# Performance work log

Hardware: AMD Instinct MI355X
Metric: run time of the kernel (lower is better)

The kernel has to match this reference:

```python
import jax, jax.numpy as jnp
import numpy as np

B, S, D, H = 4, 1024, 1024, 16
DH = D // H  # head dim = 64


def setup_inputs() -> dict:
    key = jax.random.key(0)
    k0, k1, k2 = jax.random.split(key, 3)
    x = jax.random.normal(k0, (B, S, D), dtype=jnp.float32)
    c_attn_w = jax.random.normal(k1, (D, 3 * D), dtype=jnp.float32) * 0.02
    c_attn_b = jnp.zeros((3 * D,), dtype=jnp.float32)
    c_proj_w = jax.random.normal(k2, (D, D), dtype=jnp.float32) * 0.02
    c_proj_b = jnp.zeros((D,), dtype=jnp.float32)
    return {"x": x, "c_attn_w": c_attn_w, "c_attn_b": c_attn_b,
            "c_proj_w": c_proj_w, "c_proj_b": c_proj_b}


def reference(x, c_attn_w, c_attn_b, c_proj_w, c_proj_b):
    b, s, d = x.shape
    # Conv1D (GPT-2 style): out = x @ W + b, fused QKV
    qkv = jnp.einsum('bsd,de->bse', x, c_attn_w) + c_attn_b
    q, k, v = jnp.split(qkv, 3, axis=-1)
    # split heads -> [b, h, s, dh]
    q = q.reshape(b, s, H, DH).transpose(0, 2, 1, 3)
    k = k.reshape(b, s, H, DH).transpose(0, 2, 1, 3)
    v = v.reshape(b, s, H, DH).transpose(0, 2, 1, 3)
    # scaled scores with causal future mask (triu above diagonal -> -inf)
    w = jnp.einsum('bhqd,bhkd->bhqk', q, k) / jnp.sqrt(jnp.asarray(DH, x.dtype))
    future = jnp.triu(jnp.ones((s, s), dtype=bool), k=1)
    w = jnp.where(future[None, None, :, :], jnp.asarray(-jnp.inf, w.dtype), w)
    p = jax.nn.softmax(w, axis=-1)
    a = jnp.einsum('bhqk,bhkd->bhqd', p, v)
    # merge heads -> [b, s, d]
    a = a.transpose(0, 2, 1, 3).reshape(b, s, d)
    # output projection (Conv1D)
    out = jnp.einsum('bsd,de->bse', a, c_proj_w) + c_proj_b
    return out
```

## Files before the change

### kernel.cpp

```cpp
#include <hip/hip_runtime.h>
#include <math.h>

#define BB 4
#define SS 1024
#define DD 1024
#define HH 16
#define DHH 64

typedef short bf16x8 __attribute__((ext_vector_type(8)));
typedef float f32x4 __attribute__((ext_vector_type(4)));

__device__ __forceinline__ unsigned short f2bf(float f) {
    unsigned u = __float_as_uint(f);
    u += 0x7fffu + ((u >> 16) & 1u);
    return (unsigned short)(u >> 16);
}

__device__ __forceinline__ void glds16(const void* g, void* l) {
    __builtin_amdgcn_global_load_lds(
        (const __attribute__((address_space(1))) unsigned int*)g,
        (__attribute__((address_space(3))) unsigned int*)l, 16, 0, 0);
}

#define WAITCNT_VM(n) (0xF70 | (n))

__device__ __forceinline__ int swz(int row, int col) {
    return ((((col >> 4) ^ (row >> 2)) & 3) << 4) | (col & 15);
}

__global__ __launch_bounds__(256) void prologue_kernel(
    const float* __restrict__ x, const float* __restrict__ w1,
    const float* __restrict__ w2, unsigned short* __restrict__ Xb,
    unsigned short* __restrict__ W1t, unsigned short* __restrict__ W2t)
{
    __shared__ float tile[64][65];
    const int bx = blockIdx.x;
    if (bx < 4096) {
        int i = bx * 256 + threadIdx.x;
        float4 v = ((const float4*)x)[i];
        ushort4 o = { f2bf(v.x), f2bf(v.y), f2bf(v.z), f2bf(v.w) };
        ((ushort4*)Xb)[i] = o;
        return;
    }
    const float* W; unsigned short* Wt; int N, n0, k0;
    if (bx < 4864) {
        int id = bx - 4096; W = w1; Wt = W1t; N = 3072;
        n0 = (id % 48) * 64; k0 = (id / 48) * 64;
    } else {
        int id = bx - 4864; W = w2; Wt = W2t; N = 1024;
        n0 = (id & 15) * 64; k0 = (id >> 4) * 64;
    }
    int c = threadIdx.x & 63, r0 = threadIdx.x >> 6;
    #pragma unroll
    for (int i = 0; i < 16; ++i) {
        int r = r0 + i * 4;
        tile[r][c] = W[(size_t)(k0 + r) * N + n0 + c];
    }
    __syncthreads();
    #pragma unroll
    for (int i = 0; i < 16; ++i) {
        int r = r0 + i * 4;
        Wt[(size_t)(n0 + r) * 1024 + k0 + c] = f2bf(tile[c][r]);
    }
}

__global__ __launch_bounds__(256) void gemm_mfma(
    const unsigned short* __restrict__ A,
    const unsigned short* __restrict__ Bt,
    const float* __restrict__ bias,
    unsigned short* __restrict__ Cout,
    unsigned short* __restrict__ Vt,
    int N, int K)
{
    __shared__ unsigned short smem[17408];

    const int t = threadIdx.x;
    const int lane = t & 63;
    const int w = t >> 6;
    const int l15 = lane & 15, quad = lane >> 4;
    const int bm = blockIdx.y * 128, bn = blockIdx.x * 128;

    const int fragoff = l15 * K + quad * 8;

    const f32x4 zero4 = {0.f, 0.f, 0.f, 0.f};
    f32x4 acc[4][4];
    #pragma unroll
    for (int i = 0; i < 4; ++i)
        #pragma unroll
        for (int j = 0; j < 4; ++j) acc[i][j] = zero4;

    const unsigned short* Abase = A  + (size_t)bm * K + fragoff;
    const unsigned short* Bbase = Bt + (size_t)bn * K + fragoff;

    const int R = K / 32;

    auto issue = [&](int k, int b) {
        #pragma unroll
        for (int g2 = 0; g2 < 2; ++g2) {
            int g = w * 2 + g2;
            glds16(Abase + (size_t)(g * 16) * K + k * 32,
                   &smem[b * 8192 + g * 512]);
            glds16(Bbase + (size_t)(g * 16) * K + k * 32,
                   &smem[b * 8192 + 4096 + g * 512]);
        }
    };

    issue(0, 0);
    for (int k = 0; k < R; ++k) {
        const int cur = k & 1;
        if (k + 1 < R) {
            issue(k + 1, cur ^ 1);
            __builtin_amdgcn_s_waitcnt(WAITCNT_VM(4));
        } else {
            __builtin_amdgcn_s_waitcnt(WAITCNT_VM(0));
        }
        __builtin_amdgcn_s_barrier();

        bf16x8 af[4], bfr[4];
        #pragma unroll
        for (int mi = 0; mi < 4; ++mi)
            af[mi] = *(const bf16x8*)&smem[cur * 8192 + ((w >> 1) * 4 + mi) * 512 + lane * 8];
        #pragma unroll
        for (int nj = 0; nj < 4; ++nj)
            bfr[nj] = *(const bf16x8*)&smem[cur * 8192 + 4096 + ((w & 1) * 4 + nj) * 512 + lane * 8];
        #pragma unroll
        for (int mi = 0; mi < 4; ++mi)
            #pragma unroll
            for (int nj = 0; nj < 4; ++nj)
                acc[mi][nj] = __builtin_amdgcn_mfma_f32_16x16x32_bf16(
                    af[mi], bfr[nj], acc[mi][nj], 0, 0, 0);

        __builtin_amdgcn_s_barrier();
    }

    const int wm = (w >> 1) * 64;
    const int wn = (w & 1) * 64;
    float bv[4];
    #pragma unroll
    for (int nj = 0; nj < 4; ++nj) bv[nj] = bias[bn + wn + nj * 16 + l15];

    if (bn >= 2048) {
        #pragma unroll
        for (int mi = 0; mi < 4; ++mi)
            #pragma unroll
            for (int nj = 0; nj < 4; ++nj)
                #pragma unroll
                for (int r = 0; r < 4; ++r)
                    smem[(wn + nj * 16 + l15) * 136 + wm + mi * 16 + quad * 4 + r] =
                        f2bf(acc[mi][nj][r] + bv[nj]);
        __syncthreads();
        int b = bm >> 10, s0 = bm & 1023;
        int h0 = (bn - 2048) >> 6;
        #pragma unroll
        for (int i = 0; i < 8; ++i) {
            int flat = i * 2048 + t * 8;
            int ci = flat >> 7;
            int s8 = flat & 127;
            int h = h0 + (ci >> 6), dh = ci & 63;
            *(bf16x8*)&Vt[(((size_t)b * 16 + h) * 64 + dh) * 1024 + s0 + s8] =
                *(const bf16x8*)&smem[ci * 136 + s8];
        }
    } else {
        #pragma unroll
        for (int mi = 0; mi < 4; ++mi)
            #pragma unroll
            for (int nj = 0; nj < 4; ++nj)
                #pragma unroll
                for (int r = 0; r < 4; ++r)
                    smem[(wm + mi * 16 + quad * 4 + r) * 128 + wn + nj * 16 + l15] =
                        f2bf(acc[mi][nj][r] + bv[nj]);
        __syncthreads();
        #pragma unroll
        for (int i = 0; i < 8; ++i) {
            int off = i * 2048 + t * 8;
            int row = off >> 7, col = off & 127;
            *(bf16x8*)&Cout[(size_t)(bm + row) * N + bn + col] = *(const bf16x8*)&smem[off];
        }
    }
}

__global__ __launch_bounds__(256) void gemm2_mfma(
    const unsigned short* __restrict__ A,
    const unsigned short* __restrict__ Bt,
    const float* __restrict__ bias,
    float* __restrict__ C,
    int N, int K)
{
    __shared__ unsigned short smem[16384];

    const int t = threadIdx.x;
    const int lane = t & 63;
    const int w = t >> 6;
    const int l15 = lane & 15, quad = lane >> 4;
    const int bm = blockIdx.y * 64, bn = blockIdx.x * 128;

    const int fragoff = l15 * K + quad * 8;

    const f32x4 zero4 = {0.f, 0.f, 0.f, 0.f};
    f32x4 acc[2][4];
    #pragma unroll
    for (int i = 0; i < 2; ++i)
        #pragma unroll
        for (int j = 0; j < 4; ++j) acc[i][j] = zero4;

    const unsigned short* Abase = A  + (size_t)bm * K + fragoff;
    const unsigned short* Bbase = Bt + (size_t)bn * K + fragoff;

    const int R = K / 32;

    auto issue = [&](int k, int b) {
        glds16(Abase + (size_t)(w * 16) * K + k * 32,
               &smem[b * 6144 + w * 512]);
        #pragma unroll
        for (int g2 = 0; g2 < 2; ++g2) {
            int g = w * 2 + g2;
            glds16(Bbase + (size_t)(g * 16) * K + k * 32,
                   &smem[b * 6144 + 2048 + g * 512]);
        }
    };

    issue(0, 0);
    for (int k = 0; k < R; ++k) {
        const int cur = k & 1;
        if (k + 1 < R) {
            issue(k + 1, cur ^ 1);
            __builtin_amdgcn_s_waitcnt(WAITCNT_VM(3));
        } else {
            __builtin_amdgcn_s_waitcnt(WAITCNT_VM(0));
        }
        __builtin_amdgcn_s_barrier();

        bf16x8 af[2], bfr[4];
        #pragma unroll
        for (int mi = 0; mi < 2; ++mi)
            af[mi] = *(const bf16x8*)&smem[cur * 6144 + ((w >> 1) * 2 + mi) * 512 + lane * 8];
        #pragma unroll
        for (int nj = 0; nj < 4; ++nj)
            bfr[nj] = *(const bf16x8*)&smem[cur * 6144 + 2048 + ((w & 1) * 4 + nj) * 512 + lane * 8];
        #pragma unroll
        for (int mi = 0; mi < 2; ++mi)
            #pragma unroll
            for (int nj = 0; nj < 4; ++nj)
                acc[mi][nj] = __builtin_amdgcn_mfma_f32_16x16x32_bf16(
                    af[mi], bfr[nj], acc[mi][nj], 0, 0, 0);

        __builtin_amdgcn_s_barrier();
    }

    const int wm = (w >> 1) * 32;
    const int wn = (w & 1) * 64;
    float bv[4];
    #pragma unroll
    for (int nj = 0; nj < 4; ++nj) bv[nj] = bias[bn + wn + nj * 16 + l15];

    float* fs = (float*)smem;
    #pragma unroll
    for (int mi = 0; mi < 2; ++mi)
        #pragma unroll
        for (int nj = 0; nj < 4; ++nj)
            #pragma unroll
            for (int r = 0; r < 4; ++r)
                fs[(wm + mi * 16 + quad * 4 + r) * 128 + wn + nj * 16 + l15] =
                    acc[mi][nj][r] + bv[nj];
    __syncthreads();
    #pragma unroll
    for (int i = 0; i < 8; ++i) {
        int off = i * 256 + t;
        int row = off >> 5, col = (off & 31) * 4;
        *(float4*)&C[(size_t)(bm + row) * N + bn + col] =
            *(const float4*)&fs[row * 128 + col];
    }
}

__device__ __forceinline__ void attn_tile_step8(
    bf16x8 q0, bf16x8 q1, float* mrow, float* lrow, f32x4* o,
    const unsigned short (*Ks)[80], const unsigned short (*VsT)[80],
    unsigned short (*Ps)[80],
    int wq, int l15, int quad, bool diag)
{
    const f32x4 zero4 = {0.f, 0.f, 0.f, 0.f};
    f32x4 s[4];
    #pragma unroll
    for (int nj = 0; nj < 4; ++nj) {
        int n = nj * 16 + l15;
        f32x4 sa = zero4;
        bf16x8 b0 = *(const bf16x8*)&Ks[n][swz(n, quad * 8)];
        bf16x8 b1 = *(const bf16x8*)&Ks[n][swz(n, 32 + quad * 8)];
        sa = __builtin_amdgcn_mfma_f32_16x16x32_bf16(q0, b0, sa, 0, 0, 0);
        sa = __builtin_amdgcn_mfma_f32_16x16x32_bf16(q1, b1, sa, 0, 0, 0);
        s[nj] = sa;
    }
    const float scale = 0.125f;
    #pragma unroll
    for (int nj = 0; nj < 4; ++nj)
        #pragma unroll
        for (int r = 0; r < 4; ++r) {
            float sv = s[nj][r] * scale;
            if (diag && (nj * 16 + l15) > (wq * 16 + quad * 4 + r)) sv = -INFINITY;
            s[nj][r] = sv;
        }

    float rmax[4];
    #pragma unroll
    for (int r = 0; r < 4; ++r)
        rmax[r] = fmaxf(fmaxf(s[0][r], s[1][r]), fmaxf(s[2][r], s[3][r]));
    #pragma unroll
    for (int off = 1; off < 16; off <<= 1)
        #pragma unroll
        for (int r = 0; r < 4; ++r)
            rmax[r] = fmaxf(rmax[r], __shfl_xor(rmax[r], off));

    float p[4][4], rs[4];
    #pragma unroll
    for (int r = 0; r < 4; ++r) {
        float mn = fmaxf(mrow[r], rmax[r]);
        float al = __expf(mrow[r] - mn);
        mrow[r] = mn;
        rs[r] = 0.f;
        #pragma unroll
        for (int nj = 0; nj < 4; ++nj) {
            p[nj][r] = __expf(s[nj][r] - mn);
            rs[r] += p[nj][r];
        }
        lrow[r] *= al;
        #pragma unroll
        for (int nj = 0; nj < 4; ++nj) o[nj][r] *= al;
    }
    #pragma unroll
    for (int off = 1; off < 16; off <<= 1)
        #pragma unroll
        for (int r = 0; r < 4; ++r)
            rs[r] += __shfl_xor(rs[r], off);
    #pragma unroll
    for (int r = 0; r < 4; ++r) lrow[r] += rs[r];

    #pragma unroll
    for (int nj = 0; nj < 4; ++nj)
        #pragma unroll
        for (int r = 0; r < 4; ++r) {
            int qloc = wq * 16 + quad * 4 + r;
            Ps[qloc][swz(qloc, nj * 16 + l15)] = f2bf(p[nj][r]);
        }

    #pragma unroll
    for (int kk = 0; kk < 2; ++kk) {
        int m = wq * 16 + l15;
        bf16x8 pa = *(const bf16x8*)&Ps[m][swz(m, kk * 32 + quad * 8)];
        #pragma unroll
        for (int nj = 0; nj < 4; ++nj) {
            int n = nj * 16 + l15;
            bf16x8 vb = *(const bf16x8*)&VsT[n][swz(n, kk * 32 + quad * 8)];
            o[nj] = __builtin_amdgcn_mfma_f32_16x16x32_bf16(pa, vb, o[nj], 0, 0, 0);
        }
    }
}

__global__ __launch_bounds__(512) void attn_mfma(
    const unsigned short* __restrict__ qkv,
    const unsigned short* __restrict__ Vt,
    unsigned short* __restrict__ aout)
{
    __shared__ unsigned short Ks[64][80];
    __shared__ unsigned short VsT[64][80];
    __shared__ unsigned short Ps[2][64][80];

    const int t = threadIdx.x;
    const int lane = t & 63;
    const int wave = t >> 6;
    const int wq = wave & 3;
    const int tile = wave >> 2;
    const int l15 = lane & 15, quad = lane >> 4;
    const int qlo = blockIdx.x;
    const int qhi = 15 - qlo;
    const int qb = tile ? qhi : qlo;
    const int bh = blockIdx.y;
    const int b = bh >> 4, h = bh & 15;
    const size_t qkvbase = (size_t)b * SS * 3072;
    const f32x4 zero4 = {0.f, 0.f, 0.f, 0.f};

    bf16x8 qf0, qf1;
    {
        const unsigned short* p = qkv + qkvbase +
            (size_t)(qb * 64 + wq * 16 + l15) * 3072 + h * 64 + quad * 8;
        qf0 = *(const bf16x8*)p;
        qf1 = *(const bf16x8*)(p + 32);
    }

    float mrow[4], lrow[4];
    f32x4 o[4];
    #pragma unroll
    for (int r = 0; r < 4; ++r) { mrow[r] = -INFINITY; lrow[r] = 0.f; }
    #pragma unroll
    for (int nj = 0; nj < 4; ++nj) o[nj] = zero4;

    for (int kb = 0; kb <= qhi; ++kb) {
        __syncthreads();
        {
            int r = t >> 3, cc = (t & 7) * 8;
            bf16x8 kv = *(const bf16x8*)&qkv[qkvbase + (size_t)(kb * 64 + r) * 3072 + 1024 + h * 64 + cc];
            *(bf16x8*)&Ks[r][swz(r, cc)] = kv;
            bf16x8 vv = *(const bf16x8*)&Vt[((size_t)bh * 64 + r) * 1024 + kb * 64 + cc];
            *(bf16x8*)&VsT[r][swz(r, cc)] = vv;
        }
        __syncthreads();

        if (kb <= qb)
            attn_tile_step8(qf0, qf1, mrow, lrow, o, Ks, VsT, Ps[tile],
                            wq, l15, quad, kb == qb);
    }

    #pragma unroll
    for (int r = 0; r < 4; ++r) {
        float inv = 1.0f / lrow[r];
        int rloc = wq * 16 + quad * 4 + r;
        size_t ob = ((size_t)b * SS + qb * 64 + rloc) * 1024 + h * 64;
        #pragma unroll
        for (int nj = 0; nj < 4; ++nj)
            aout[ob + nj * 16 + l15] = f2bf(o[nj][r] * inv);
    }
}

extern "C" void kernel_launch(void* const* d_in, const int* in_sizes, int n_in,
                              void* d_out, int out_size, void* d_ws, size_t ws_size,
                              hipStream_t stream)
{
    const float* x     = (const float*)d_in[0];
    const float* wqkv  = (const float*)d_in[1];
    const float* bqkv  = (const float*)d_in[2];
    const float* wproj = (const float*)d_in[3];
    const float* bproj = (const float*)d_in[4];
    float* out = (float*)d_out;

    unsigned short* ws   = (unsigned short*)d_ws;
    unsigned short* Xb   = ws;
    unsigned short* W1t  = Xb  + (size_t)4096 * 1024;
    unsigned short* W2t  = W1t + (size_t)3072 * 1024;
    unsigned short* qkv  = W2t + (size_t)1024 * 1024;
    unsigned short* Vt   = qkv + (size_t)4096 * 3072;
    unsigned short* abuf = Vt  + (size_t)64 * 64 * 1024;

    prologue_kernel<<<5120, 256, 0, stream>>>(x, wqkv, wproj, Xb, W1t, W2t);

    gemm_mfma<<<dim3(3072 / 128, 4096 / 128), 256, 0, stream>>>(
        Xb, W1t, bqkv, qkv, Vt, 3072, 1024);

    attn_mfma<<<dim3(8, 64), 512, 0, stream>>>(qkv, Vt, abuf);

    gemm2_mfma<<<dim3(1024 / 128, 4096 / 64), 256, 0, stream>>>(
        abuf, W2t, bproj, out, 1024, 1024);
}
```

Measured before the change: 198.7 us.

## Double-buffer attention K/V tiles via async global-to-LDS loads in fragment layout

Replaces the synchronous register-staged K and V^T tile loads in the attention kernel with global_load_lds DMA into a double-buffered LDS area, prefetching the next key block while the current one is computed. The LDS layout is changed so each MFMA operand fragment is stored contiguously per lane, which removes the swizzled indexing on reads. This is meant to hide global load latency and cut VGPR staging and address math, at the cost of doubling the K/V shared memory and relying on manual waitcnt/barrier placement for correctness.

```diff
diff --git a/kernel.cpp b/kernel.cpp
--- a/kernel.cpp
+++ b/kernel.cpp
@@ -272,22 +272,21 @@
     }
 }
 
-__device__ __forceinline__ void attn_tile_step8(
+__device__ __forceinline__ void attn_step8(
     bf16x8 q0, bf16x8 q1, float* mrow, float* lrow, f32x4* o,
-    const unsigned short (*Ks)[80], const unsigned short (*VsT)[80],
-    unsigned short (*Ps)[80],
-    int wq, int l15, int quad, bool diag)
+    const unsigned short* __restrict__ KV,
+    unsigned short (* __restrict__ Ps)[80],
+    int wq, int lane, int l15, int quad, bool diag)
 {
     const f32x4 zero4 = {0.f, 0.f, 0.f, 0.f};
     f32x4 s[4];
     #pragma unroll
     for (int nj = 0; nj < 4; ++nj) {
-        int n = nj * 16 + l15;
         f32x4 sa = zero4;
-        bf16x8 b0 = *(const bf16x8*)&Ks[n][swz(n, quad * 8)];
-        bf16x8 b1 = *(const bf16x8*)&Ks[n][swz(n, 32 + quad * 8)];
-        sa = __builtin_amdgcn_mfma_f32_16x16x32_bf16(q0, b0, sa, 0, 0, 0);
-        sa = __builtin_amdgcn_mfma_f32_16x16x32_bf16(q1, b1, sa, 0, 0, 0);
+        sa = __builtin_amdgcn_mfma_f32_16x16x32_bf16(
+            q0, *(const bf16x8*)&KV[(nj * 2 + 0) * 512 + lane * 8], sa, 0, 0, 0);
+        sa = __builtin_amdgcn_mfma_f32_16x16x32_bf16(
+            q1, *(const bf16x8*)&KV[(nj * 2 + 1) * 512 + lane * 8], sa, 0, 0, 0);
         s[nj] = sa;
     }
     const float scale = 0.125f;
@@ -347,11 +346,10 @@
         int m = wq * 16 + l15;
         bf16x8 pa = *(const bf16x8*)&Ps[m][swz(m, kk * 32 + quad * 8)];
         #pragma unroll
-        for (int nj = 0; nj < 4; ++nj) {
-            int n = nj * 16 + l15;
-            bf16x8 vb = *(const bf16x8*)&VsT[n][swz(n, kk * 32 + quad * 8)];
-            o[nj] = __builtin_amdgcn_mfma_f32_16x16x32_bf16(pa, vb, o[nj], 0, 0, 0);
-        }
+        for (int nj = 0; nj < 4; ++nj)
+            o[nj] = __builtin_amdgcn_mfma_f32_16x16x32_bf16(
+                pa, *(const bf16x8*)&KV[(8 + nj * 2 + kk) * 512 + lane * 8],
+                o[nj], 0, 0, 0);
     }
 }
 
@@ -360,8 +358,7 @@
     const unsigned short* __restrict__ Vt,
     unsigned short* __restrict__ aout)
 {
-    __shared__ unsigned short Ks[64][80];
-    __shared__ unsigned short VsT[64][80];
+    __shared__ unsigned short KV[2][16 * 512];
     __shared__ unsigned short Ps[2][64][80];
 
     const int t = threadIdx.x;
@@ -376,6 +373,8 @@
     const int bh = blockIdx.y;
     const int b = bh >> 4, h = bh & 15;
     const size_t qkvbase = (size_t)b * SS * 3072;
+    const unsigned short* kbase = qkv + qkvbase + 1024 + h * 64;
+    const unsigned short* vbase = Vt + (size_t)bh * 64 * 1024;
     const f32x4 zero4 = {0.f, 0.f, 0.f, 0.f};
 
     bf16x8 qf0, qf1;
@@ -386,6 +385,14 @@
         qf1 = *(const bf16x8*)(p + 32);
     }
 
+    const int sg = wave >> 1, skk = wave & 1;
+    auto issue = [&](int kb, int buf) {
+        glds16(kbase + (size_t)(kb * 64 + sg * 16 + l15) * 3072 + skk * 32 + quad * 8,
+               &KV[buf][wave * 512]);
+        glds16(vbase + (size_t)(sg * 16 + l15) * 1024 + kb * 64 + skk * 32 + quad * 8,
+               &KV[buf][(8 + wave) * 512]);
+    };
+
     float mrow[4], lrow[4];
     f32x4 o[4];
     #pragma unroll
@@ -393,20 +400,22 @@
     #pragma unroll
     for (int nj = 0; nj < 4; ++nj) o[nj] = zero4;
 
+    issue(0, 0);
     for (int kb = 0; kb <= qhi; ++kb) {
-        __syncthreads();
-        {
-            int r = t >> 3, cc = (t & 7) * 8;
-            bf16x8 kv = *(const bf16x8*)&qkv[qkvbase + (size_t)(kb * 64 + r) * 3072 + 1024 + h * 64 + cc];
-            *(bf16x8*)&Ks[r][swz(r, cc)] = kv;
-            bf16x8 vv = *(const bf16x8*)&Vt[((size_t)bh * 64 + r) * 1024 + kb * 64 + cc];
-            *(bf16x8*)&VsT[r][swz(r, cc)] = vv;
-        }
-        __syncthreads();
+        const int cur = kb & 1;
+        if (kb < qhi) {
+            issue(kb + 1, cur ^ 1);
+            __builtin_amdgcn_s_waitcnt(WAITCNT_VM(2));
+        } else {
+            __builtin_amdgcn_s_waitcnt(WAITCNT_VM(0));
+        }
+        __builtin_amdgcn_s_barrier();
 
         if (kb <= qb)
-            attn_tile_step8(qf0, qf1, mrow, lrow, o, Ks, VsT, Ps[tile],
-                            wq, l15, quad, kb == qb);
+            attn_step8(qf0, qf1, mrow, lrow, o, KV[cur], Ps[tile],
+                       wq, lane, l15, quad, kb == qb);
+
+        __builtin_amdgcn_s_barrier();
     }
 
     #pragma unroll
```

Result: slower. 207.1 us (+4.3%).
